# Kernel optimization log

Measured on AMD Instinct MI355X. Metric: run time of the kernel, lower is better.

Reference implementation:

```python
import jax, jax.numpy as jnp
import numpy as np

B, L, H, D = 4, 2048, 8, 64


def _combined_mask(Lq):
    # True = masked (disallowed), matching masked_fill_(mask, -inf)
    i = jnp.arange(Lq)[:, None]
    j = jnp.arange(Lq)[None, :]
    diff = i - j
    # log-sparse: query i attends to itself and positions at power-of-2 offsets back
    pow2 = (diff > 0) & ((diff & (diff - 1)) == 0)
    allowed = (diff == 0) | pow2
    log_mask = ~allowed
    causal = j > i  # TriangularCausalMask: strictly-upper triangle masked
    return log_mask | causal  # [Lq, Lq]


def setup_inputs() -> dict:
    key = jax.random.key(0)
    kq, kk, kv = jax.random.split(key, 3)
    return {
        "queries": jax.random.normal(kq, (B, L, H, D), jnp.float32),
        "keys": jax.random.normal(kk, (B, L, H, D), jnp.float32),
        "values": jax.random.normal(kv, (B, L, H, D), jnp.float32),
    }


def reference(queries, keys, values):
    Bq, Lq, Hh, Dd = queries.shape
    scale = 1.0 / jnp.sqrt(jnp.asarray(Dd, queries.dtype))
    # dense scores [B,H,L,L], then structured log-sparse + causal masking
    scores = jnp.einsum('blhd,bshd->bhls', queries, keys)
    mask = _combined_mask(Lq)  # [L,L] True = masked
    scores = jnp.where(mask[None, None, :, :], -jnp.inf, scores)
    A = jax.nn.softmax(scale * scores, axis=-1)  # scale*(-inf) stays -inf
    # dropout is identity in eval mode (reference baseline)
    V = jnp.einsum('bhls,bshd->blhd', A, values)
    return V
```

## Files before the change

### kernel.cpp

```cpp
#include <hip/hip_runtime.h>


constexpr int B = 4, L = 2048, H = 8, D = 64;
constexpr int NPOS = 12;

__global__ __launch_bounds__(256) void logsparse_attn_kernel(
    const float* __restrict__ Q, const float* __restrict__ K,
    const float* __restrict__ V, float* __restrict__ O) {
  const int wid  = (blockIdx.x * blockDim.x + threadIdx.x) >> 6;
  const int lane = threadIdx.x & 63;
  const int g    = lane >> 4;
  const int dsub = lane & 15;

  const int bi    = wid >> 1;
  const int hbase = (wid & 1) * 4;
  const int i     = bi & (L - 1);

  const size_t base = ((size_t)bi * H + (hbase + g)) * D + dsub * 4;

  const float4 q4 = *reinterpret_cast<const float4*>(Q + base);

  float sc[NPOS];
  #pragma unroll
  for (int t = 0; t < NPOS; ++t) {
    const int off    = (t == 0) ? 0 : (1 << (t - 1));
    const bool valid = (off <= i);
    const size_t kb  = valid ? (base - (size_t)off * (H * D)) : base;
    const float4 k4  = *reinterpret_cast<const float4*>(K + kb);
    float p = q4.x * k4.x + q4.y * k4.y + q4.z * k4.z + q4.w * k4.w;
    p += __shfl_xor(p, 1, 64);
    p += __shfl_xor(p, 2, 64);
    p += __shfl_xor(p, 4, 64);
    p += __shfl_xor(p, 8, 64);
    sc[t] = valid ? p * 0.125f : -INFINITY;
  }

  float m = sc[0];
  #pragma unroll
  for (int t = 1; t < NPOS; ++t) m = fmaxf(m, sc[t]);
  float denom = 0.f;
  #pragma unroll
  for (int t = 0; t < NPOS; ++t) {
    sc[t] = __expf(sc[t] - m);
    denom += sc[t];
  }
  const float inv = 1.0f / denom;

  float4 acc = make_float4(0.f, 0.f, 0.f, 0.f);
  #pragma unroll
  for (int t = 0; t < NPOS; ++t) {
    const int off    = (t == 0) ? 0 : (1 << (t - 1));
    const bool valid = (off <= i);
    const size_t vb  = valid ? (base - (size_t)off * (H * D)) : base;
    const float4 v4  = *reinterpret_cast<const float4*>(V + vb);
    acc.x += sc[t] * v4.x;
    acc.y += sc[t] * v4.y;
    acc.z += sc[t] * v4.z;
    acc.w += sc[t] * v4.w;
  }
  acc.x *= inv; acc.y *= inv; acc.z *= inv; acc.w *= inv;
  *reinterpret_cast<float4*>(O + base) = acc;
}

extern "C" void kernel_launch(void* const* d_in, const int* in_sizes, int n_in,
                              void* d_out, int out_size, void* d_ws, size_t ws_size,
                              hipStream_t stream) {
  const float* Q = (const float*)d_in[0];
  const float* K = (const float*)d_in[1];
  const float* V = (const float*)d_in[2];
  float* O = (float*)d_out;

  const int rows    = B * L * H;
  const int waves   = rows / 4;
  const int threads = 256;
  const int blocks  = (waves * 64) / threads;
  logsparse_attn_kernel<<<blocks, threads, 0, stream>>>(Q, K, V, O);
}
```

Before: 102.6 us.

## Prefetch all K/V rows upfront, swizzle workgroups, use nontemporal Q/O access

All twelve K and V float4 loads are issued before any compute, so the V loads no longer wait behind the softmax and there is more memory-level parallelism. The wave-to-row mapping is remapped so each half of the heads is processed as a contiguous sweep, and the block index is swizzled across eight groups, likely to spread work across XCDs and improve L2 reuse of nearby K/V rows. Q loads and O stores use nontemporal hints to avoid polluting cache. Holding 24 float4 values raises register pressure.

```diff
diff --git a/kernel.cpp b/kernel.cpp
--- a/kernel.cpp
+++ b/kernel.cpp
@@ -1,38 +1,53 @@
 #include <hip/hip_runtime.h>
 
 
+typedef float f32x4 __attribute__((ext_vector_type(4)));
+
 constexpr int B = 4, L = 2048, H = 8, D = 64;
 constexpr int NPOS = 12;
+constexpr int NWG  = (B * L * 2 * 64) / 256;
 
 __global__ __launch_bounds__(256) void logsparse_attn_kernel(
     const float* __restrict__ Q, const float* __restrict__ K,
     const float* __restrict__ V, float* __restrict__ O) {
-  const int wid  = (blockIdx.x * blockDim.x + threadIdx.x) >> 6;
+  const int bid = blockIdx.x;
+  const int swz = (bid & 7) * (NWG / 8) + (bid >> 3);
+  const int wid = swz * 4 + (int)(threadIdx.x >> 6);
   const int lane = threadIdx.x & 63;
   const int g    = lane >> 4;
   const int dsub = lane & 15;
 
-  const int bi    = wid >> 1;
-  const int hbase = (wid & 1) * 4;
-  const int i     = bi & (L - 1);
+  const int half = wid >> 13;
+  const int bi   = wid & 8191;
+  const int i    = bi & (L - 1);
+  const int hbase = half * 4;
 
   const size_t base = ((size_t)bi * H + (hbase + g)) * D + dsub * 4;
 
-  const float4 q4 = *reinterpret_cast<const float4*>(Q + base);
+  const f32x4 q4 = __builtin_nontemporal_load(
+      reinterpret_cast<const f32x4*>(Q + base));
+
+  f32x4 kx[NPOS], vx[NPOS];
+  #pragma unroll
+  for (int t = 0; t < NPOS; ++t) {
+    const int off    = (t == 0) ? 0 : (1 << (t - 1));
+    const bool valid = (off <= i);
+    const size_t rb  = valid ? (base - (size_t)off * (H * D)) : base;
+    kx[t] = *reinterpret_cast<const f32x4*>(K + rb);
+    vx[t] = *reinterpret_cast<const f32x4*>(V + rb);
+  }
 
   float sc[NPOS];
   #pragma unroll
   for (int t = 0; t < NPOS; ++t) {
-    const int off    = (t == 0) ? 0 : (1 << (t - 1));
-    const bool valid = (off <= i);
-    const size_t kb  = valid ? (base - (size_t)off * (H * D)) : base;
-    const float4 k4  = *reinterpret_cast<const float4*>(K + kb);
-    float p = q4.x * k4.x + q4.y * k4.y + q4.z * k4.z + q4.w * k4.w;
+    float p = q4.x * kx[t].x + q4.y * kx[t].y
+            + q4.z * kx[t].z + q4.w * kx[t].w;
     p += __shfl_xor(p, 1, 64);
     p += __shfl_xor(p, 2, 64);
     p += __shfl_xor(p, 4, 64);
     p += __shfl_xor(p, 8, 64);
-    sc[t] = valid ? p * 0.125f : -INFINITY;
+    const int off = (t == 0) ? 0 : (1 << (t - 1));
+    sc[t] = (off <= i) ? p * 0.125f : -INFINITY;
   }
 
   float m = sc[0];
@@ -46,20 +61,16 @@
   }
   const float inv = 1.0f / denom;
 
-  float4 acc = make_float4(0.f, 0.f, 0.f, 0.f);
+  f32x4 acc = {0.f, 0.f, 0.f, 0.f};
   #pragma unroll
   for (int t = 0; t < NPOS; ++t) {
-    const int off    = (t == 0) ? 0 : (1 << (t - 1));
-    const bool valid = (off <= i);
-    const size_t vb  = valid ? (base - (size_t)off * (H * D)) : base;
-    const float4 v4  = *reinterpret_cast<const float4*>(V + vb);
-    acc.x += sc[t] * v4.x;
-    acc.y += sc[t] * v4.y;
-    acc.z += sc[t] * v4.z;
-    acc.w += sc[t] * v4.w;
+    acc.x += sc[t] * vx[t].x;
+    acc.y += sc[t] * vx[t].y;
+    acc.z += sc[t] * vx[t].z;
+    acc.w += sc[t] * vx[t].w;
   }
   acc.x *= inv; acc.y *= inv; acc.z *= inv; acc.w *= inv;
-  *reinterpret_cast<float4*>(O + base) = acc;
+  __builtin_nontemporal_store(acc, reinterpret_cast<f32x4*>(O + base));
 }
 
 extern "C" void kernel_launch(void* const* d_in, const int* in_sizes, int n_in,
@@ -70,9 +81,5 @@
   const float* V = (const float*)d_in[2];
   float* O = (float*)d_out;
 
-  const int rows    = B * L * H;
-  const int waves   = rows / 4;
-  const int threads = 256;
-  const int blocks  = (waves * 64) / threads;
-  logsparse_attn_kernel<<<blocks, threads, 0, stream>>>(Q, K, V, O);
+  logsparse_attn_kernel<<<NWG, 256, 0, stream>>>(Q, K, V, O);
 }
```

Result: no change. 102.4 us (-0.2%).
